# Performance work log

Measured on AMD Instinct MI355X. Metric: run time of the kernel, lower is better.

The kernel has to match this reference:

```python
import jax, jax.numpy as jnp
import numpy as np
from jax import lax

NPOINT = 1024
NSAMPLE = 32
BN_EPS = 1e-3  # keras BatchNormalization default epsilon


def _fps(xyz, npoint):
    # Farthest point sampling. Matches the TF loop: the NEW farthest index is
    # recorded at each step (the initial index-0 seed is never recorded).
    B, N, _ = xyz.shape

    def step(carry, _):
        dist, far = carry
        centroid = jnp.take_along_axis(xyz, far[:, None, None], axis=1)  # (B,1,3)
        d2 = jnp.sum(jnp.square(xyz - centroid), axis=-1)  # (B,N)
        dist = jnp.minimum(dist, d2)
        nf = jnp.argmax(dist, axis=-1).astype(jnp.int32)
        return (dist, nf), nf

    init = (jnp.full((B, N), 1e10, dtype=xyz.dtype), jnp.zeros((B,), jnp.int32))
    _, idxs = lax.scan(step, init, None, length=npoint)
    return jnp.transpose(idxs)  # (B, npoint)


def _pairwise_d2(a, b):
    # a: (B,S,3), b: (B,N,3) -> (B,S,N) squared distances
    a2 = jnp.sum(a * a, axis=-1, keepdims=True)
    b2 = jnp.sum(b * b, axis=-1, keepdims=True)
    ab = jnp.einsum('bsc,bnc->bsn', a, b)
    return jnp.maximum(a2 - 2.0 * ab + jnp.swapaxes(b2, 1, 2), 0.0)


def _forward(xyz, features, params):
    fps_idx = _fps(xyz, NPOINT)  # (B,S)
    new_xyz = jnp.take_along_axis(xyz, fps_idx[..., None], axis=1)  # (B,S,3)
    d2 = _pairwise_d2(new_xyz, xyz)  # (B,S,N)
    _, idx = lax.top_k(-d2, NSAMPLE)  # (B,S,K) knn indices
    gather = jax.vmap(lambda p, i: p[i])  # per-batch gather
    grouped_xyz = gather(xyz, idx) - new_xyz[:, :, None, :]  # (B,S,K,3)
    grouped_feat = gather(features, idx)  # (B,S,K,C)
    x = jnp.concatenate([grouped_xyz, grouped_feat], axis=-1)
    for W, b, g, be, m, v in params:
        # Conv2D(kernel=1, activation='relu') then BatchNormalization (inference)
        x = jax.nn.relu(jnp.einsum('bskc,cd->bskd', x, W) + b)
        x = g * (x - m) * lax.rsqrt(v + BN_EPS) + be
    return new_xyz, jnp.max(x, axis=2)  # (B,S,3), (B,S,C_out)


def setup_inputs() -> dict:
    key = jax.random.key(0)
    ks = jax.random.split(key, 16)
    B, N, CF = 16, 4096, 64
    mlp = [64, 64, 128]
    inp = {
        'xyz': jax.random.normal(ks[0], (B, N, 3), jnp.float32),
        'features': jax.random.normal(ks[1], (B, N, CF), jnp.float32),
    }
    c = 3 + CF
    ki = 2
    for li, co in enumerate(mlp):
        inp[f'W{li}'] = jax.random.normal(ks[ki], (c, co), jnp.float32) * 0.05; ki += 1
        inp[f'b{li}'] = jnp.zeros((co,), jnp.float32)
        inp[f'g{li}'] = 1.0 + 0.02 * jax.random.normal(ks[ki], (co,), jnp.float32); ki += 1
        inp[f'be{li}'] = 0.02 * jax.random.normal(ks[ki], (co,), jnp.float32); ki += 1
        inp[f'm{li}'] = jnp.zeros((co,), jnp.float32)
        inp[f'v{li}'] = jnp.ones((co,), jnp.float32)
        c = co
    return inp


def reference(xyz, features, W0, b0, g0, be0, m0, v0, W1, b1, g1, be1, m1, v1, W2, b2, g2, be2, m2, v2):
    params = [(W0, b0, g0, be0, m0, v0), (W1, b1, g1, be1, m1, v1), (W2, b2, g2, be2, m2, v2)]
    return _forward(xyz, features, params)
```

## Files before the change

kernel.cpp:

```cpp
#include <hip/hip_runtime.h>

#define NB 16
#define NPTS 4096
#define NS 1024
#define NK 32
#define NCF 64


#define F_INF __int_as_float(0x7f800000)

#define DPP_SHR1   0x111
#define DPP_SHR2   0x112
#define DPP_SHR4   0x114
#define DPP_SHR8   0x118
#define DPP_BCAST15 0x142
#define DPP_BCAST31 0x143

#define DPP_MAX_STEP(cur, CTRL) do{ \
  int lo_=__builtin_amdgcn_update_dpp((int)(unsigned)(cur),(int)(unsigned)(cur),CTRL,0xF,0xF,false); \
  int hi_=__builtin_amdgcn_update_dpp((int)(unsigned)((cur)>>32),(int)(unsigned)((cur)>>32),CTRL,0xF,0xF,false); \
  unsigned long long nk_=(((unsigned long long)(unsigned)hi_)<<32)|(unsigned)lo_; \
  if (nk_>(cur)) (cur)=nk_; \
}while(0)

__global__ __launch_bounds__(256, 2) void fps_kernel(
  const float* __restrict__ xyz, float* __restrict__ out)
{
  __shared__ float sxyz[NPTS*3];
  __shared__ unsigned long long skey[2][4];
  __shared__ int sfps[NS];
  const int b = blockIdx.x, tid = threadIdx.x;
  const float* bp = xyz + (size_t)b*NPTS*3;

  {
    const float4* src=(const float4*)bp;
    float4* dst=(float4*)sxyz;
    for (int i=tid;i<NPTS*3/4;i+=256) dst[i]=src[i];
  }
  float px[16],py[16],pz[16],dist[16];
  #pragma unroll
  for (int r=0;r<16;r++){
    int p=r*256+tid;
    px[r]=bp[p*3]; py[r]=bp[p*3+1]; pz[r]=bp[p*3+2];
    dist[r]=1e10f;
  }
  __syncthreads();
  int far=0;
  for (int s=0;s<NS;++s){
    float cx=sxyz[far*3],cy=sxyz[far*3+1],cz=sxyz[far*3+2];
    float bv=-1.0f; int bslot=0;
    #pragma unroll
    for (int r=0;r<16;r++){
      float dx=__fsub_rn(px[r],cx);
      float dy=__fsub_rn(py[r],cy);
      float dz=__fsub_rn(pz[r],cz);
      float d2=__fadd_rn(__fadd_rn(__fmul_rn(dx,dx),__fmul_rn(dy,dy)),__fmul_rn(dz,dz));
      float nd=fminf(dist[r],d2);
      dist[r]=nd;
      if (nd>bv){bv=nd;bslot=r;}
    }
    int bidx=bslot*256+tid;
    unsigned long long cur=(((unsigned long long)__float_as_uint(bv))<<32)
                           |(unsigned)(4095-bidx);
    DPP_MAX_STEP(cur,DPP_SHR1);
    DPP_MAX_STEP(cur,DPP_SHR2);
    DPP_MAX_STEP(cur,DPP_SHR4);
    DPP_MAX_STEP(cur,DPP_SHR8);
    DPP_MAX_STEP(cur,DPP_BCAST15);
    DPP_MAX_STEP(cur,DPP_BCAST31);
    const int par=s&1;
    if ((tid&63)==63) skey[par][tid>>6]=cur;
    __syncthreads();
    unsigned long long m=skey[par][0];
    #pragma unroll
    for (int w=1;w<4;w++){ unsigned long long o=skey[par][w]; if (o>m) m=o; }
    far=4095-(int)(m&0xFFFFFFFFu);
    if (tid==0) sfps[s]=far;
  }
  __syncthreads();
  for (int s=tid;s<NS;s+=256){
    int p=sfps[s];
    size_t o=((size_t)b*NS+s)*3;
    out[o]=sxyz[p*3]; out[o+1]=sxyz[p*3+1]; out[o+2]=sxyz[p*3+2];
  }
}

__global__ __launch_bounds__(256, 4) void knn_kernel(
  const float* __restrict__ xyz, const float* __restrict__ newxyz,
  float* __restrict__ out2)
{
  __shared__ float sdump[256*33];
  __shared__ float sl1[64*33];
  __shared__ float sTq[16];
  __shared__ int   sE[16];
  __shared__ int   sCnt[16];
  __shared__ int   sTCnt[16];
  __shared__ int   sIdx[16][32];
  __shared__ int   sTie[16][48];
  const int tid=threadIdx.x;
  const int wave=tid>>6, lane=tid&63;
  const int qw=lane>>4;
  const int part=lane&15;
  const int ql=wave*4+qw;
  const int gq=blockIdx.x*16+ql;
  const int b=gq>>10;
  const float* base=xyz+(size_t)b*NPTS*3;

  float ax=newxyz[(size_t)gq*3],ay=newxyz[(size_t)gq*3+1],az=newxyz[(size_t)gq*3+2];
  float a2=__fadd_rn(__fadd_rn(__fmul_rn(ax,ax),__fmul_rn(ay,ay)),__fmul_rn(az,az));

  float kD[NK];
  #pragma unroll
  for (int p=0;p<NK;p++) kD[p]=F_INF;

  #pragma unroll 2
  for (int t=0;t<NPTS/16;++t){
    int n=(t<<4)|part;
    float bx=base[n*3],by=base[n*3+1],bz=base[n*3+2];
    float b2=__fadd_rn(__fadd_rn(__fmul_rn(bx,bx),__fmul_rn(by,by)),__fmul_rn(bz,bz));
    float ab=__fadd_rn(__fadd_rn(__fmul_rn(ax,bx),__fmul_rn(ay,by)),__fmul_rn(az,bz));
    float tt=__fadd_rn(__fsub_rn(a2,__fmul_rn(2.0f,ab)),b2);
    float d2=fmaxf(tt,0.0f);
    #pragma unroll
    for (int p=NK-1;p>0;--p)
      kD[p]=__builtin_amdgcn_fmed3f(kD[p-1],d2,kD[p]);
    kD[0]=fminf(kD[0],d2);
  }

  #pragma unroll
  for (int p=0;p<NK;p++) sdump[tid*33+p]=kD[p];
  __syncthreads();

  if (tid<64){
    int qq=tid>>2, g=tid&3;
    int rbase=(qq>>2)*64+(qq&3)*16+g*4;
    const float* r0=sdump+(size_t)(rbase+0)*33;
    const float* r1=sdump+(size_t)(rbase+1)*33;
    const float* r2=sdump+(size_t)(rbase+2)*33;
    const float* r3=sdump+(size_t)(rbase+3)*33;
    float* o=sl1+(size_t)tid*33;
    int h0=0,h1=0,h2=0,h3=0;
    float c0=r0[0],c1=r1[0],c2=r2[0],c3=r3[0];
    #pragma unroll 1
    for (int i=0;i<NK;++i){
      bool s01=c1<c0; float m01=s01?c1:c0;
      bool s23=c3<c2; float m23=s23?c3:c2;
      bool sm=m23<m01; float m=sm?m23:m01;
      o[i]=m;
      int w=sm?(s23?3:2):(s01?1:0);
      if (w==0){h0++; c0=(h0<NK)?r0[h0]:F_INF;}
      else if (w==1){h1++; c1=(h1<NK)?r1[h1]:F_INF;}
      else if (w==2){h2++; c2=(h2<NK)?r2[h2]:F_INF;}
      else {h3++; c3=(h3<NK)?r3[h3]:F_INF;}
    }
  }
  __syncthreads();

  if (tid<16){
    const float* r0=sl1+(size_t)(tid*4+0)*33;
    const float* r1=sl1+(size_t)(tid*4+1)*33;
    const float* r2=sl1+(size_t)(tid*4+2)*33;
    const float* r3=sl1+(size_t)(tid*4+3)*33;
    int h0=0,h1=0,h2=0,h3=0;
    float c0=r0[0],c1=r1[0],c2=r2[0],c3=r3[0];
    float prev=-1.0f; int run=0;
    #pragma unroll 1
    for (int i=0;i<NK;++i){
      bool s01=c1<c0; float m01=s01?c1:c0;
      bool s23=c3<c2; float m23=s23?c3:c2;
      bool sm=m23<m01; float m=sm?m23:m01;
      if (m==prev) run++; else {prev=m; run=1;}
      int w=sm?(s23?3:2):(s01?1:0);
      if (w==0){h0++; c0=(h0<NK)?r0[h0]:F_INF;}
      else if (w==1){h1++; c1=(h1<NK)?r1[h1]:F_INF;}
      else if (w==2){h2++; c2=(h2<NK)?r2[h2]:F_INF;}
      else {h3++; c3=(h3<NK)?r3[h3]:F_INF;}
    }
    sTq[tid]=prev; sE[tid]=run;
    sCnt[tid]=0; sTCnt[tid]=0;
  }
  __syncthreads();

  {
    const float Tq=sTq[ql];
    #pragma unroll 2
    for (int t=0;t<NPTS/16;++t){
      int n=(t<<4)|part;
      float bx=base[n*3],by=base[n*3+1],bz=base[n*3+2];
      float b2=__fadd_rn(__fadd_rn(__fmul_rn(bx,bx),__fmul_rn(by,by)),__fmul_rn(bz,bz));
      float ab=__fadd_rn(__fadd_rn(__fmul_rn(ax,bx),__fmul_rn(ay,by)),__fmul_rn(az,bz));
      float tt=__fadd_rn(__fsub_rn(a2,__fmul_rn(2.0f,ab)),b2);
      float d2=fmaxf(tt,0.0f);
      if (d2<Tq){
        int pos=atomicAdd(&sCnt[ql],1);
        if (pos<32) sIdx[ql][pos]=n;
      } else if (d2==Tq){
        int tp=atomicAdd(&sTCnt[ql],1);
        if (tp<48) sTie[ql][tp]=n;
      }
    }
  }
  __syncthreads();

  if (tid<16){
    int e=sE[tid], c=sCnt[tid];
    int tn=sTCnt[tid]; if (tn>48) tn=48;
    for (int j=0;j<e;++j){
      int bm=0x7FFFFFFF, bi=0;
      for (int i=0;i<tn;++i){ int v=sTie[tid][i]; if (v<bm){bm=v;bi=i;} }
      sTie[tid][bi]=0x7FFFFFFF;
      if (c+j<32) sIdx[tid][c+j]=bm;
    }
  }
  __syncthreads();

  for (int i=tid;i<512;i+=256){
    int q=i>>5, k=i&31;
    out2[(size_t)(blockIdx.x*16+q)*128+k]=__int_as_float(sIdx[q][k]);
  }
}

__global__ __launch_bounds__(128, 3) void mlp_kernel(
  const float* __restrict__ feat, const float* __restrict__ xyz,
  const float* __restrict__ newxyz,
  const float* __restrict__ W0,const float* __restrict__ b0,
  const float* __restrict__ g0,const float* __restrict__ be0,
  const float* __restrict__ m0,const float* __restrict__ v0,
  const float* __restrict__ W1,const float* __restrict__ b1,
  const float* __restrict__ g1,const float* __restrict__ be1,
  const float* __restrict__ m1,const float* __restrict__ v1,
  const float* __restrict__ W2,const float* __restrict__ b2,
  const float* __restrict__ g2,const float* __restrict__ be2,
  const float* __restrict__ m2,const float* __restrict__ v2,
  float* __restrict__ out2)
{
  __shared__ float sX[128*67];
  const int tid=threadIdx.x;
  const int q=blockIdx.x*4+(tid>>5);
  const int k=tid&31;
  const int b=q>>10;
  const int pt=__float_as_int(out2[(size_t)q*128+k]);

  float* myx=sX+tid*67;
  {
    const float* nx=newxyz+(size_t)q*3;
    const float* pp=xyz+((size_t)b*NPTS+pt)*3;
    myx[0]=pp[0]-nx[0]; myx[1]=pp[1]-nx[1]; myx[2]=pp[2]-nx[2];
    const float4* fp=(const float4*)(feat+((size_t)b*NPTS+pt)*NCF);
    #pragma unroll
    for (int i=0;i<16;i++){
      float4 u=fp[i]; float* d=myx+3+i*4;
      d[0]=u.x; d[1]=u.y; d[2]=u.z; d[3]=u.w;
    }
  }
  float acc[64];
  #pragma unroll
  for (int c=0;c<64;c++) acc[c]=b0[c];
  #pragma unroll 2
  for (int j=0;j<67;++j){
    float xj=myx[j];
    const float4* wr=(const float4*)(W0+j*64);
    #pragma unroll
    for (int c4=0;c4<16;c4++){
      float4 w=wr[c4];
      acc[c4*4+0]=fmaf(xj,w.x,acc[c4*4+0]);
      acc[c4*4+1]=fmaf(xj,w.y,acc[c4*4+1]);
      acc[c4*4+2]=fmaf(xj,w.z,acc[c4*4+2]);
      acc[c4*4+3]=fmaf(xj,w.w,acc[c4*4+3]);
    }
  }
  #pragma unroll
  for (int c=0;c<64;c++){
    float A=g0[c]*rsqrtf(v0[c]+1e-3f);
    myx[c]=fmaf(A,fmaxf(acc[c],0.0f),be0[c]-m0[c]*A);
  }
  #pragma unroll
  for (int c=0;c<64;c++) acc[c]=b1[c];
  #pragma unroll 2
  for (int j=0;j<64;++j){
    float xj=myx[j];
    const float4* wr=(const float4*)(W1+j*64);
    #pragma unroll
    for (int c4=0;c4<16;c4++){
      float4 w=wr[c4];
      acc[c4*4+0]=fmaf(xj,w.x,acc[c4*4+0]);
      acc[c4*4+1]=fmaf(xj,w.y,acc[c4*4+1]);
      acc[c4*4+2]=fmaf(xj,w.z,acc[c4*4+2]);
      acc[c4*4+3]=fmaf(xj,w.w,acc[c4*4+3]);
    }
  }
  #pragma unroll
  for (int c=0;c<64;c++){
    float A=g1[c]*rsqrtf(v1[c]+1e-3f);
    myx[c]=fmaf(A,fmaxf(acc[c],0.0f),be1[c]-m1[c]*A);
  }
  #pragma unroll 1
  for (int ch=0;ch<2;++ch){
    const int co=ch*64;
    #pragma unroll
    for (int c=0;c<64;c++) acc[c]=b2[co+c];
    #pragma unroll 2
    for (int j=0;j<64;++j){
      float xj=myx[j];
      const float4* wr=(const float4*)(W2+j*128+co);
      #pragma unroll
      for (int c4=0;c4<16;c4++){
        float4 w=wr[c4];
        acc[c4*4+0]=fmaf(xj,w.x,acc[c4*4+0]);
        acc[c4*4+1]=fmaf(xj,w.y,acc[c4*4+1]);
        acc[c4*4+2]=fmaf(xj,w.z,acc[c4*4+2]);
        acc[c4*4+3]=fmaf(xj,w.w,acc[c4*4+3]);
      }
    }
    #pragma unroll
    for (int c=0;c<64;c++){
      float A=g2[co+c]*rsqrtf(v2[co+c]+1e-3f);
      float v=fmaf(A,fmaxf(acc[c],0.0f),be2[co+c]-m2[co+c]*A);
      v=fmaxf(v,__shfl_xor(v,1));
      v=fmaxf(v,__shfl_xor(v,2));
      v=fmaxf(v,__shfl_xor(v,4));
      v=fmaxf(v,__shfl_xor(v,8));
      v=fmaxf(v,__shfl_xor(v,16));
      acc[c]=v;
    }
    if (k==0){
      float4* op=(float4*)(out2+(size_t)q*128+co);
      #pragma unroll
      for (int c=0;c<64;c+=4)
        op[c/4]=make_float4(acc[c],acc[c+1],acc[c+2],acc[c+3]);
    }
  }
}

extern "C" void kernel_launch(void* const* d_in, const int* in_sizes, int n_in,
                              void* d_out, int out_size, void* d_ws, size_t ws_size,
                              hipStream_t stream)
{
  const float* xyz=(const float*)d_in[0];
  const float* feat=(const float*)d_in[1];
  float* out=(float*)d_out;
  float* out2=out+(size_t)NB*NS*3;
  (void)d_ws; (void)ws_size;

  fps_kernel<<<NB,256,0,stream>>>(xyz,out);
  knn_kernel<<<NB*NS/16,256,0,stream>>>(xyz,out,out2);
  mlp_kernel<<<NB*NS/4,128,0,stream>>>(feat,xyz,out,
    (const float*)d_in[2],(const float*)d_in[3],
    (const float*)d_in[4],(const float*)d_in[5],
    (const float*)d_in[6],(const float*)d_in[7],
    (const float*)d_in[8],(const float*)d_in[9],
    (const float*)d_in[10],(const float*)d_in[11],
    (const float*)d_in[12],(const float*)d_in[13],
    (const float*)d_in[14],(const float*)d_in[15],
    (const float*)d_in[16],(const float*)d_in[17],
    (const float*)d_in[18],(const float*)d_in[19],
    out2);
}
```

Measured before the change: 1.345 ms.

## Pack xyz to float4, widen FPS blocks to 512 threads, re-read points each step

Adds a pack kernel that writes xyz as float4 into the output buffer as scratch. The FPS kernel now runs 512 threads with 8 points per thread, and each step re-reads the points from global memory instead of keeping them in registers. The per-thread argmax becomes a tree reduction, and the cross-wave reduction covers 8 waves. This is meant to double the threads working on the serial FPS loop, but every one of the 1024 steps now issues global loads, which may hit cache but adds latency. The reused output region is overwritten later by knn.

```diff
diff --git a/kernel.cpp b/kernel.cpp
--- a/kernel.cpp
+++ b/kernel.cpp
@@ -23,43 +23,52 @@
   if (nk_>(cur)) (cur)=nk_; \
 }while(0)
 
-__global__ __launch_bounds__(256, 2) void fps_kernel(
-  const float* __restrict__ xyz, float* __restrict__ out)
-{
-  __shared__ float sxyz[NPTS*3];
-  __shared__ unsigned long long skey[2][4];
+__global__ void pack_kernel(const float* __restrict__ xyz, float4* __restrict__ pk)
+{
+  int i=blockIdx.x*1024+threadIdx.x;
+  if (i<NB*NPTS)
+    pk[i]=make_float4(xyz[(size_t)i*3],xyz[(size_t)i*3+1],xyz[(size_t)i*3+2],0.0f);
+}
+
+__global__ __launch_bounds__(512, 2) void fps_kernel(
+  const float4* __restrict__ pk, float* __restrict__ out)
+{
+  __shared__ float4 sp[NPTS];
+  __shared__ unsigned long long skey[2][8];
   __shared__ int sfps[NS];
-  const int b = blockIdx.x, tid = threadIdx.x;
-  const float* bp = xyz + (size_t)b*NPTS*3;
-
-  {
-    const float4* src=(const float4*)bp;
-    float4* dst=(float4*)sxyz;
-    for (int i=tid;i<NPTS*3/4;i+=256) dst[i]=src[i];
-  }
-  float px[16],py[16],pz[16],dist[16];
-  #pragma unroll
-  for (int r=0;r<16;r++){
-    int p=r*256+tid;
-    px[r]=bp[p*3]; py[r]=bp[p*3+1]; pz[r]=bp[p*3+2];
-    dist[r]=1e10f;
-  }
-  __syncthreads();
-  int far=0;
+  const int b=blockIdx.x, tid=threadIdx.x;
+  const int wave=tid>>6, lane=tid&63;
+  const float4* bpk=pk+(size_t)b*NPTS;
+
+  for (int i=tid;i<NPTS;i+=512) sp[i]=bpk[i];
+  float dist[8];
+  #pragma unroll
+  for (int r=0;r<8;r++) dist[r]=1e10f;
+  __syncthreads();
+
+  float4 cseed=sp[0];
+  float cx=cseed.x, cy=cseed.y, cz=cseed.z;
   for (int s=0;s<NS;++s){
-    float cx=sxyz[far*3],cy=sxyz[far*3+1],cz=sxyz[far*3+2];
-    float bv=-1.0f; int bslot=0;
-    #pragma unroll
-    for (int r=0;r<16;r++){
-      float dx=__fsub_rn(px[r],cx);
-      float dy=__fsub_rn(py[r],cy);
-      float dz=__fsub_rn(pz[r],cz);
+    #pragma unroll
+    for (int r=0;r<8;r++){
+      float4 q=bpk[r*512+tid];
+      float dx=__fsub_rn(q.x,cx);
+      float dy=__fsub_rn(q.y,cy);
+      float dz=__fsub_rn(q.z,cz);
       float d2=__fadd_rn(__fadd_rn(__fmul_rn(dx,dx),__fmul_rn(dy,dy)),__fmul_rn(dz,dz));
-      float nd=fminf(dist[r],d2);
-      dist[r]=nd;
-      if (nd>bv){bv=nd;bslot=r;}
-    }
-    int bidx=bslot*256+tid;
+      dist[r]=fminf(dist[r],d2);
+    }
+    float v4_[4]; int s4_[4];
+    #pragma unroll
+    for (int i=0;i<4;i++){ bool g=dist[2*i+1]>dist[2*i]; v4_[i]=g?dist[2*i+1]:dist[2*i]; s4_[i]=g?(2*i+1):(2*i); }
+    float v2_[2]; int s2_[2];
+    #pragma unroll
+    for (int i=0;i<2;i++){ bool g=v4_[2*i+1]>v4_[2*i]; v2_[i]=g?v4_[2*i+1]:v4_[2*i]; s2_[i]=g?s4_[2*i+1]:s4_[2*i]; }
+    bool gf=v2_[1]>v2_[0];
+    float bv=gf?v2_[1]:v2_[0];
+    int bslot=gf?s2_[1]:s2_[0];
+
+    int bidx=bslot*512+tid;
     unsigned long long cur=(((unsigned long long)__float_as_uint(bv))<<32)
                            |(unsigned)(4095-bidx);
     DPP_MAX_STEP(cur,DPP_SHR1);
@@ -69,19 +78,24 @@
     DPP_MAX_STEP(cur,DPP_BCAST15);
     DPP_MAX_STEP(cur,DPP_BCAST31);
     const int par=s&1;
-    if ((tid&63)==63) skey[par][tid>>6]=cur;
+    if (lane==63) skey[par][wave]=cur;
     __syncthreads();
-    unsigned long long m=skey[par][0];
-    #pragma unroll
-    for (int w=1;w<4;w++){ unsigned long long o=skey[par][w]; if (o>m) m=o; }
-    far=4095-(int)(m&0xFFFFFFFFu);
+    unsigned long long k0=skey[par][0],k1=skey[par][1],k2=skey[par][2],k3=skey[par][3];
+    unsigned long long k4=skey[par][4],k5=skey[par][5],k6=skey[par][6],k7=skey[par][7];
+    unsigned long long a0=k0>k1?k0:k1, a1=k2>k3?k2:k3, a2=k4>k5?k4:k5, a3=k6>k7?k6:k7;
+    unsigned long long b0=a0>a1?a0:a1, b1=a2>a3?a2:a3;
+    unsigned long long m=b0>b1?b0:b1;
+    int far=4095-(int)(m&0xFFFFFFFFu);
+    float4 cc=sp[far];
+    cx=cc.x; cy=cc.y; cz=cc.z;
     if (tid==0) sfps[s]=far;
   }
   __syncthreads();
-  for (int s=tid;s<NS;s+=256){
+  for (int s=tid;s<NS;s+=512){
     int p=sfps[s];
     size_t o=((size_t)b*NS+s)*3;
-    out[o]=sxyz[p*3]; out[o+1]=sxyz[p*3+1]; out[o+2]=sxyz[p*3+2];
+    float4 pp=sp[p];
+    out[o]=pp.x; out[o+1]=pp.y; out[o+2]=pp.z;
   }
 }
 
@@ -340,9 +354,11 @@
   const float* feat=(const float*)d_in[1];
   float* out=(float*)d_out;
   float* out2=out+(size_t)NB*NS*3;
+  float4* pk=(float4*)out2;
   (void)d_ws; (void)ws_size;
 
-  fps_kernel<<<NB,256,0,stream>>>(xyz,out);
+  pack_kernel<<<(NB*NPTS+1023)/1024,1024,0,stream>>>(xyz,pk);
+  fps_kernel<<<NB,512,0,stream>>>(pk,out);
   knn_kernel<<<NB*NS/16,256,0,stream>>>(xyz,out,out2);
   mlp_kernel<<<NB*NS/4,128,0,stream>>>(feat,xyz,out,
     (const float*)d_in[2],(const float*)d_in[3],
```

After: 1.411 ms. +4.9%, slower.

## Split MLP output channels across two lanes per neighbor to halve registers

Applied to the files above, without the earlier changes.

The MLP kernel now uses 256 threads per block, with two lanes per grouped neighbor. Each lane computes half of every layer's output channels, so per-thread accumulators drop from 64 to 32 floats. The gathered features are loaded cooperatively and block barriers are added between layers, because each half now reads channels written by the other. The aim is more parallelism and occupancy in exchange for twice the threads, the extra barriers and shared-memory reads repeated by both halves.

```diff
diff --git a/kernel.cpp b/kernel.cpp
--- a/kernel.cpp
+++ b/kernel.cpp
@@ -220,7 +220,7 @@
   }
 }
 
-__global__ __launch_bounds__(128, 3) void mlp_kernel(
+__global__ __launch_bounds__(256, 4) void mlp_kernel(
   const float* __restrict__ feat, const float* __restrict__ xyz,
   const float* __restrict__ newxyz,
   const float* __restrict__ W0,const float* __restrict__ b0,
@@ -236,32 +236,40 @@
 {
   __shared__ float sX[128*67];
   const int tid=threadIdx.x;
-  const int q=blockIdx.x*4+(tid>>5);
-  const int k=tid&31;
+  const int ql=tid>>6;
+  const int lane=tid&63;
+  const int k=lane&31;
+  const int h=lane>>5;
+  const int q=blockIdx.x*4+ql;
   const int b=q>>10;
   const int pt=__float_as_int(out2[(size_t)q*128+k]);
 
-  float* myx=sX+tid*67;
+  float* myx=sX+(size_t)(ql*32+k)*67;
   {
     const float* nx=newxyz+(size_t)q*3;
     const float* pp=xyz+((size_t)b*NPTS+pt)*3;
-    myx[0]=pp[0]-nx[0]; myx[1]=pp[1]-nx[1]; myx[2]=pp[2]-nx[2];
+    if (h==0){
+      myx[0]=pp[0]-nx[0]; myx[1]=pp[1]-nx[1]; myx[2]=pp[2]-nx[2];
+    }
     const float4* fp=(const float4*)(feat+((size_t)b*NPTS+pt)*NCF);
     #pragma unroll
-    for (int i=0;i<16;i++){
-      float4 u=fp[i]; float* d=myx+3+i*4;
+    for (int i=0;i<8;i++){
+      float4 u=fp[h*8+i]; float* d=myx+3+(h*8+i)*4;
       d[0]=u.x; d[1]=u.y; d[2]=u.z; d[3]=u.w;
     }
   }
-  float acc[64];
-  #pragma unroll
-  for (int c=0;c<64;c++) acc[c]=b0[c];
+  __syncthreads();
+
+  float acc[32];
+  const int co0=h*32;
+  #pragma unroll
+  for (int c=0;c<32;c++) acc[c]=b0[co0+c];
   #pragma unroll 2
   for (int j=0;j<67;++j){
     float xj=myx[j];
-    const float4* wr=(const float4*)(W0+j*64);
-    #pragma unroll
-    for (int c4=0;c4<16;c4++){
+    const float4* wr=(const float4*)(W0+j*64+co0);
+    #pragma unroll
+    for (int c4=0;c4<8;c4++){
       float4 w=wr[c4];
       acc[c4*4+0]=fmaf(xj,w.x,acc[c4*4+0]);
       acc[c4*4+1]=fmaf(xj,w.y,acc[c4*4+1]);
@@ -270,18 +278,19 @@
     }
   }
   #pragma unroll
-  for (int c=0;c<64;c++){
-    float A=g0[c]*rsqrtf(v0[c]+1e-3f);
-    myx[c]=fmaf(A,fmaxf(acc[c],0.0f),be0[c]-m0[c]*A);
-  }
-  #pragma unroll
-  for (int c=0;c<64;c++) acc[c]=b1[c];
+  for (int c=0;c<32;c++){
+    float A=g0[co0+c]*rsqrtf(v0[co0+c]+1e-3f);
+    myx[co0+c]=fmaf(A,fmaxf(acc[c],0.0f),be0[co0+c]-m0[co0+c]*A);
+  }
+  __syncthreads();
+  #pragma unroll
+  for (int c=0;c<32;c++) acc[c]=b1[co0+c];
   #pragma unroll 2
   for (int j=0;j<64;++j){
     float xj=myx[j];
-    const float4* wr=(const float4*)(W1+j*64);
-    #pragma unroll
-    for (int c4=0;c4<16;c4++){
+    const float4* wr=(const float4*)(W1+j*64+co0);
+    #pragma unroll
+    for (int c4=0;c4<8;c4++){
       float4 w=wr[c4];
       acc[c4*4+0]=fmaf(xj,w.x,acc[c4*4+0]);
       acc[c4*4+1]=fmaf(xj,w.y,acc[c4*4+1]);
@@ -290,21 +299,22 @@
     }
   }
   #pragma unroll
-  for (int c=0;c<64;c++){
-    float A=g1[c]*rsqrtf(v1[c]+1e-3f);
-    myx[c]=fmaf(A,fmaxf(acc[c],0.0f),be1[c]-m1[c]*A);
-  }
+  for (int c=0;c<32;c++){
+    float A=g1[co0+c]*rsqrtf(v1[co0+c]+1e-3f);
+    myx[co0+c]=fmaf(A,fmaxf(acc[c],0.0f),be1[co0+c]-m1[co0+c]*A);
+  }
+  __syncthreads();
   #pragma unroll 1
   for (int ch=0;ch<2;++ch){
-    const int co=ch*64;
-    #pragma unroll
-    for (int c=0;c<64;c++) acc[c]=b2[co+c];
+    const int cb=ch*64+co0;
+    #pragma unroll
+    for (int c=0;c<32;c++) acc[c]=b2[cb+c];
     #pragma unroll 2
     for (int j=0;j<64;++j){
       float xj=myx[j];
-      const float4* wr=(const float4*)(W2+j*128+co);
+      const float4* wr=(const float4*)(W2+j*128+cb);
       #pragma unroll
-      for (int c4=0;c4<16;c4++){
+      for (int c4=0;c4<8;c4++){
         float4 w=wr[c4];
         acc[c4*4+0]=fmaf(xj,w.x,acc[c4*4+0]);
         acc[c4*4+1]=fmaf(xj,w.y,acc[c4*4+1]);
@@ -313,9 +323,9 @@
       }
     }
     #pragma unroll
-    for (int c=0;c<64;c++){
-      float A=g2[co+c]*rsqrtf(v2[co+c]+1e-3f);
-      float v=fmaf(A,fmaxf(acc[c],0.0f),be2[co+c]-m2[co+c]*A);
+    for (int c=0;c<32;c++){
+      float A=g2[cb+c]*rsqrtf(v2[cb+c]+1e-3f);
+      float v=fmaf(A,fmaxf(acc[c],0.0f),be2[cb+c]-m2[cb+c]*A);
       v=fmaxf(v,__shfl_xor(v,1));
       v=fmaxf(v,__shfl_xor(v,2));
       v=fmaxf(v,__shfl_xor(v,4));
@@ -324,9 +334,9 @@
       acc[c]=v;
     }
     if (k==0){
-      float4* op=(float4*)(out2+(size_t)q*128+co);
+      float4* op=(float4*)(out2+(size_t)q*128+cb);
       #pragma unroll
-      for (int c=0;c<64;c+=4)
+      for (int c=0;c<32;c+=4)
         op[c/4]=make_float4(acc[c],acc[c+1],acc[c+2],acc[c+3]);
     }
   }
@@ -344,7 +354,7 @@
 
   fps_kernel<<<NB,256,0,stream>>>(xyz,out);
   knn_kernel<<<NB*NS/16,256,0,stream>>>(xyz,out,out2);
-  mlp_kernel<<<NB*NS/4,128,0,stream>>>(feat,xyz,out,
+  mlp_kernel<<<NB*NS/4,256,0,stream>>>(feat,xyz,out,
     (const float*)d_in[2],(const float*)d_in[3],
     (const float*)d_in[4],(const float*)d_in[5],
     (const float*)d_in[6],(const float*)d_in[7],
```

Result: slower. 1.946 ms (+44.7%).
